# Optimization experiments

Measured on AMD Instinct MI355X. Metric: run time of the kernel, lower is better.

The kernel has to match this reference:

```python
import jax, jax.numpy as jnp
import numpy as np

N_RBF = 32
EPS_DIST = 0.01
R_RBF_MAX = 5.0
POWERS = (1.0, -1.0)


def _rbf_features(dist):
    # dist: [..., ] -> [..., N_RBF]; Gaussian-on-distance 'soft one-hot'
    q = jnp.linspace(0.0, 1.0, N_RBF).astype(dist.dtype)
    mu = q ** 2 * R_RBF_MAX
    sigma = (1.0 + R_RBF_MAX * q) / 7.0
    d = dist[..., None]
    return d ** 2 * jnp.exp(-d - ((d - mu) / sigma) ** 2)


def _pair_features(diff, dist):
    # RBF (32) + distance powers (2) + raw differences (3) = 37 features
    f_dist = jnp.stack(
        [dist ** n if n > 0 else 1.0 / (dist ** (-n) + EPS_DIST) for n in POWERS],
        axis=-1,
    )
    return jnp.concatenate([_rbf_features(dist), f_dist, diff], axis=-1)


def _mlp(x, Ws, bs):
    # MLP with linear_out=False: activation applied after every layer incl. last
    for W, b in zip(Ws, bs):
        x = jax.nn.silu(x @ W + b)
    return x


def setup_inputs() -> dict:
    key = jax.random.key(0)
    ks = jax.random.split(key, 6)
    B, N, M = 2048, 32, 8
    D_PAIR = N_RBF + 2 + 3  # 37
    H, F1, F_ION = 128, 128, 32
    r = jax.random.normal(ks[0], (B, N, 3), jnp.float32) * 2.0
    R = jax.random.normal(ks[1], (M, 3), jnp.float32) * 3.0
    Z = jnp.arange(1, M + 1, dtype=jnp.float32)
    init = lambda k, s: (jax.random.normal(k, s, jnp.float32) / np.sqrt(s[0])).astype(jnp.float32)
    return dict(
        r=r, R=R, Z=Z,
        W0=init(ks[2], (D_PAIR, H)), b0=jnp.zeros((H,), jnp.float32),
        W1=init(ks[3], (H, F1)), b1=jnp.zeros((F1,), jnp.float32),
        Wion=init(ks[4], (1, F_ION)), bion=jnp.zeros((F_ION,), jnp.float32),
    )


def reference(r, R, Z, W0, b0, W1, b1, Wion, bion):
    B, N = r.shape[0], r.shape[1]
    # --- pairwise diffs / distances ---
    diff_el_el = r[..., :, None, :] - r[..., None, :, :]          # [B,N,N,3]
    eye = jnp.eye(N, dtype=r.dtype)
    # safe sqrt on the diagonal (grad-safe), diagonal distance forced to 0
    dist_el_el = jnp.sqrt(jnp.sum(diff_el_el ** 2, axis=-1) + eye) * (1.0 - eye)  # [B,N,N]
    diff_el_ion = r[..., :, None, :] - R                           # [B,N,M,3]
    dist_el_ion = jnp.sqrt(jnp.sum(diff_el_ion ** 2, axis=-1))     # [B,N,M]

    # --- per-edge features ---
    features_el_el = _pair_features(diff_el_el, dist_el_el)        # [B,N,N,37]
    features_el_ion = _pair_features(diff_el_ion, dist_el_ion)     # [B,N,M,37]

    # --- edge MLP + sum aggregation over ions ---
    h = _mlp(features_el_ion, [W0, W1], [b0, b1])                  # [B,N,M,128]
    one_el = jnp.sum(h, axis=-2)                                   # [B,N,128]
    concat_ei = jnp.reshape(features_el_ion, features_el_ion.shape[:-2] + (-1,))  # [B,N,M*37]
    features_el = jnp.concatenate([one_el, concat_ei], axis=-1)    # [B,N,128+M*37]

    # --- ion features ---
    Zt = jnp.tile(Z, (B, 1))                                       # [B,M]
    features_ion = jax.nn.silu(Zt[..., None] @ Wion + bion)        # [B,M,32]
    return (features_el, features_ion)
```

## Files before the change

### kernel.cpp

```cpp
#include <hip/hip_runtime.h>


typedef __attribute__((ext_vector_type(8))) short short8;
typedef __attribute__((ext_vector_type(4))) float f32x4;

#define ITERS     8
#define UNITS_IT  16
#define ROWLEN    424
#define OUT_EL    27787264

__device__ __forceinline__ unsigned short f2bf(float f){
    unsigned int u = __builtin_bit_cast(unsigned int, f);
    u += 0x7fffu + ((u >> 16) & 1u);
    return (unsigned short)(u >> 16);
}
__device__ __forceinline__ unsigned int cvtpk_bf16(float lo, float hi){
    unsigned int r;
    asm("v_cvt_pk_bf16_f32 %0, %1, %2" : "=v"(r) : "v"(lo), "v"(hi));
    return r;
}
__device__ __forceinline__ unsigned short bf16s(float x){
    return (unsigned short)cvtpk_bf16(x, x);
}
__device__ __forceinline__ float fast_silu(float x){
    return x * __builtin_amdgcn_rcpf(1.0f + __expf(-x));
}

__global__ __launch_bounds__(512, 4)
void el_kernel(const float* __restrict__ r,
               const float* __restrict__ Rion,
               const float* __restrict__ W0,
               const float* __restrict__ b0,
               const float* __restrict__ W1,
               const float* __restrict__ b1,
               const float* __restrict__ Z,
               const float* __restrict__ Wion,
               const float* __restrict__ bion,
               float* __restrict__ out)
{
    __shared__ __align__(16) unsigned short W0L[8][2][64][8];
    __shared__ __align__(16) unsigned short W1L[8][4][64][8];
    __shared__ __align__(16) unsigned short UNI[8][2048];

    const int t    = threadIdx.x;
    const int lane = t & 63;
    const int w    = t >> 6;
    const int quad = lane >> 4;
    const int l16  = lane & 15;

    for (int i = t; i < 8*2*64*8; i += 512){
        int j = i & 7, ln = (i >> 3) & 63, ch = (i >> 9) & 1, tc = i >> 10;
        int q = ln >> 4, n = tc*16 + (ln & 15);
        float v = 0.f;
        if (ch == 0)            v = W0[(q*8 + j)*128 + n];
        else if (q == 0){
            if      (j < 5)     v = W0[(32 + j)*128 + n];
            else if (j == 5)    v = b0[n];
        }
        ((unsigned short*)W0L)[i] = f2bf(v);
    }
    for (int i = t; i < 8*4*64*8; i += 512){
        int j = i & 7, ln = (i >> 3) & 63, c = (i >> 9) & 3, tc = i >> 11;
        int k = c*32 + (ln >> 4)*8 + j, n = tc*16 + (ln & 15);
        ((unsigned short*)W1L)[i] = f2bf(W1[k*128 + n]);
    }
    if (t < 128){
        UNI[t >> 4][512 + (t & 15)*8 + 5] = 0x3F80;
        UNI[t >> 4][512 + (t & 15)*8 + 6] = 0;
        UNI[t >> 4][512 + (t & 15)*8 + 7] = 0;
    }

    {
        int e0 = (blockIdx.x*512 + t)*2;
        int j0 = e0 & 31, mm = (e0 >> 5) & 7;
        float z = Z[mm];
        float2 v;
        v.x = fast_silu(z * Wion[j0]     + bion[j0]);
        v.y = fast_silu(z * Wion[j0 + 1] + bion[j0 + 1]);
        *(float2*)&out[OUT_EL + e0] = v;
    }

    const int frow  = t >> 2;
    const int phase = t & 3;
    const int ul    = frow >> 3;
    const int m     = frow & 7;
    const int e16   = frow & 15;
    const float Rx = Rion[m*3+0];
    const float Ry = Rion[m*3+1];
    const float Rz = Rion[m*3+2];

    unsigned short* const uw = &UNI[w][0];
    const int h0row = l16 * 128;
    const int swz   = (l16 & 7) << 3;

    const f32x4 zeroc = {0.f,0.f,0.f,0.f};

    float bias1[8];
    #pragma unroll
    for (int tc = 0; tc < 8; ++tc) bias1[tc] = b1[tc*16 + l16];

    float muA[8], isA[8];
    #pragma unroll
    for (int k = 0; k < 8; ++k){
        float q = (float)(phase + 4*k) * (1.0f/31.0f);
        muA[k] = q*q*5.0f;
        isA[k] = 7.0f * __builtin_amdgcn_rcpf(1.0f + 5.0f*q);
    }

    const int ubase0 = blockIdx.x * (UNITS_IT * ITERS);

    float cx, cy, cz;
    {
        int gu = ubase0 + ul;
        cx = r[gu*3+0]; cy = r[gu*3+1]; cz = r[gu*3+2];
    }

    __syncthreads();

    for (int it = 0; it < ITERS; ++it){
        const int ubase = ubase0 + it * UNITS_IT;

        float nx = 0.f, ny = 0.f, nz = 0.f;
        if (it < ITERS-1){
            int gun = ubase + UNITS_IT + ul;
            nx = r[gun*3+0]; ny = r[gun*3+1]; nz = r[gun*3+2];
        }

        {
            int gu = ubase + ul;
            float dx = cx - Rx;
            float dy = cy - Ry;
            float dz = cz - Rz;
            float d2 = dx*dx + dy*dy + dz*dz;
            float d  = __builtin_amdgcn_sqrtf(d2);
            float* orow = &out[(size_t)gu*ROWLEN + 128 + m*37];
            #pragma unroll
            for (int k = 0; k < 8; ++k){
                float uu  = (d - muA[k]) * isA[k];
                float val = d2 * __expf(-d - uu*uu);
                orow[phase + 4*k] = val;
                uw[(k >> 1)*128 + e16*8 + phase + ((k & 1) << 2)] = bf16s(val);
            }
            if (phase == 0){
                orow[32] = d;  uw[512 + e16*8 + 0] = bf16s(d);
                orow[36] = dz; uw[512 + e16*8 + 4] = bf16s(dz);
            } else if (phase == 1){
                float v = __builtin_amdgcn_rcpf(d + 0.01f);
                orow[33] = v;  uw[512 + e16*8 + 1] = bf16s(v);
            } else if (phase == 2){
                orow[34] = dx; uw[512 + e16*8 + 2] = bf16s(dx);
            } else {
                orow[35] = dy; uw[512 + e16*8 + 3] = bf16s(dy);
                uw[512 + e16*8 + 5] = 0x3F80;
            }
        }

        short8 bf0 = *(const short8*)&uw[quad*128 + l16*8];
        short8 bf1 = *(const short8*)&uw[512 + l16*8];
        #pragma unroll
        for (int tc = 0; tc < 8; ++tc){
            short8 a0 = *(const short8*)&W0L[tc][0][lane][0];
            short8 a1 = *(const short8*)&W0L[tc][1][lane][0];
            f32x4 acc = __builtin_amdgcn_mfma_f32_16x16x32_bf16(a0, bf0, zeroc, 0, 0, 0);
            acc       = __builtin_amdgcn_mfma_f32_16x16x32_bf16(a1, bf1, acc,   0, 0, 0);
            unsigned int p01 = cvtpk_bf16(fast_silu(acc[0]), fast_silu(acc[1]));
            unsigned int p23 = cvtpk_bf16(fast_silu(acc[2]), fast_silu(acc[3]));
            unsigned long long pk = (unsigned long long)p01 |
                                    ((unsigned long long)p23 << 32);
            *(unsigned long long*)&uw[h0row + ((tc*16 + quad*4) ^ swz)] = pk;
        }

        short8 afk[4];
        #pragma unroll
        for (int c = 0; c < 4; ++c)
            afk[c] = *(const short8*)&uw[h0row + ((c*32 + quad*8) ^ swz)];

        f32x4 acc1[8];
        #pragma unroll
        for (int i = 0; i < 8; ++i) acc1[i] = zeroc;
        __builtin_amdgcn_s_setprio(1);
        #pragma unroll
        for (int c = 0; c < 4; ++c){
            #pragma unroll
            for (int tc = 0; tc < 8; ++tc){
                short8 bw = *(const short8*)&W1L[tc][c][lane][0];
                acc1[tc] = __builtin_amdgcn_mfma_f32_16x16x32_bf16(afk[c], bw, acc1[tc], 0, 0, 0);
            }
        }
        __builtin_amdgcn_s_setprio(0);
        #pragma unroll
        for (int tc = 0; tc < 8; ++tc){
            float v = 0.f;
            #pragma unroll
            for (int rr = 0; rr < 4; ++rr) v += fast_silu(acc1[tc][rr] + bias1[tc]);
            v += __shfl_xor(v, 16, 64);
            if ((quad & 1) == 0){
                size_t gu = (size_t)(ubase + 2*w + (quad >> 1));
                out[gu*ROWLEN + tc*16 + l16] = v;
            }
        }

        cx = nx; cy = ny; cz = nz;
    }
}

extern "C" void kernel_launch(void* const* d_in, const int* in_sizes, int n_in,
                              void* d_out, int out_size, void* d_ws, size_t ws_size,
                              hipStream_t stream)
{
    const float* r    = (const float*)d_in[0];
    const float* Rion = (const float*)d_in[1];
    const float* Z    = (const float*)d_in[2];
    const float* W0   = (const float*)d_in[3];
    const float* b0   = (const float*)d_in[4];
    const float* W1   = (const float*)d_in[5];
    const float* b1   = (const float*)d_in[6];
    const float* Wion = (const float*)d_in[7];
    const float* bion = (const float*)d_in[8];
    float* out = (float*)d_out;

    el_kernel<<<dim3(512), dim3(512), 0, stream>>>(r, Rion, W0, b0, W1, b1,
                                                   Z, Wion, bion, out);
}
```

Baseline: 181.6 us.

## Double block size and stream hidden layer in chunks to shrink LDS

Blocks grow to 1024 threads (16 waves), with 32 units per iteration over 4 iterations. The two MLP layers are interleaved per 32-column chunk, so each chunk of the first-layer output goes through a small per-wave LDS scratch and straight into the second-layer MFMAs. This cuts the per-wave LDS buffer from 2048 to 640 shorts. The RBF constants are recomputed inline instead of being kept in registers, and the ion-feature tail now writes one element per thread. The aim is higher occupancy and less LDS and register use, at the cost of a tighter register budget from the new launch bounds (possible spills) and a scratch area that overlaps the feature staging region.

```diff
diff --git a/kernel.cpp b/kernel.cpp
--- a/kernel.cpp
+++ b/kernel.cpp
@@ -4,8 +4,8 @@
 typedef __attribute__((ext_vector_type(8))) short short8;
 typedef __attribute__((ext_vector_type(4))) float f32x4;
 
-#define ITERS     8
-#define UNITS_IT  16
+#define ITERS     4
+#define UNITS_IT  32
 #define ROWLEN    424
 #define OUT_EL    27787264
 
@@ -26,7 +26,7 @@
     return x * __builtin_amdgcn_rcpf(1.0f + __expf(-x));
 }
 
-__global__ __launch_bounds__(512, 4)
+__global__ __launch_bounds__(1024, 8)
 void el_kernel(const float* __restrict__ r,
                const float* __restrict__ Rion,
                const float* __restrict__ W0,
@@ -40,7 +40,7 @@
 {
     __shared__ __align__(16) unsigned short W0L[8][2][64][8];
     __shared__ __align__(16) unsigned short W1L[8][4][64][8];
-    __shared__ __align__(16) unsigned short UNI[8][2048];
+    __shared__ __align__(16) unsigned short UNI[16][640];
 
     const int t    = threadIdx.x;
     const int lane = t & 63;
@@ -48,7 +48,7 @@
     const int quad = lane >> 4;
     const int l16  = lane & 15;
 
-    for (int i = t; i < 8*2*64*8; i += 512){
+    for (int i = t; i < 8*2*64*8; i += 1024){
         int j = i & 7, ln = (i >> 3) & 63, ch = (i >> 9) & 1, tc = i >> 10;
         int q = ln >> 4, n = tc*16 + (ln & 15);
         float v = 0.f;
@@ -59,25 +59,21 @@
         }
         ((unsigned short*)W0L)[i] = f2bf(v);
     }
-    for (int i = t; i < 8*4*64*8; i += 512){
+    for (int i = t; i < 8*4*64*8; i += 1024){
         int j = i & 7, ln = (i >> 3) & 63, c = (i >> 9) & 3, tc = i >> 11;
         int k = c*32 + (ln >> 4)*8 + j, n = tc*16 + (ln & 15);
         ((unsigned short*)W1L)[i] = f2bf(W1[k*128 + n]);
     }
-    if (t < 128){
+    if (t < 256){
         UNI[t >> 4][512 + (t & 15)*8 + 5] = 0x3F80;
         UNI[t >> 4][512 + (t & 15)*8 + 6] = 0;
         UNI[t >> 4][512 + (t & 15)*8 + 7] = 0;
     }
 
     {
-        int e0 = (blockIdx.x*512 + t)*2;
-        int j0 = e0 & 31, mm = (e0 >> 5) & 7;
-        float z = Z[mm];
-        float2 v;
-        v.x = fast_silu(z * Wion[j0]     + bion[j0]);
-        v.y = fast_silu(z * Wion[j0 + 1] + bion[j0 + 1]);
-        *(float2*)&out[OUT_EL + e0] = v;
+        int e = blockIdx.x*1024 + t;
+        int j = e & 31, mm = (e >> 5) & 7;
+        out[OUT_EL + e] = fast_silu(Z[mm] * Wion[j] + bion[j]);
     }
 
     const int frow  = t >> 2;
@@ -90,22 +86,12 @@
     const float Rz = Rion[m*3+2];
 
     unsigned short* const uw = &UNI[w][0];
-    const int h0row = l16 * 128;
-    const int swz   = (l16 & 7) << 3;
 
     const f32x4 zeroc = {0.f,0.f,0.f,0.f};
 
     float bias1[8];
     #pragma unroll
     for (int tc = 0; tc < 8; ++tc) bias1[tc] = b1[tc*16 + l16];
-
-    float muA[8], isA[8];
-    #pragma unroll
-    for (int k = 0; k < 8; ++k){
-        float q = (float)(phase + 4*k) * (1.0f/31.0f);
-        muA[k] = q*q*5.0f;
-        isA[k] = 7.0f * __builtin_amdgcn_rcpf(1.0f + 5.0f*q);
-    }
 
     const int ubase0 = blockIdx.x * (UNITS_IT * ITERS);
 
@@ -136,7 +122,10 @@
             float* orow = &out[(size_t)gu*ROWLEN + 128 + m*37];
             #pragma unroll
             for (int k = 0; k < 8; ++k){
-                float uu  = (d - muA[k]) * isA[k];
+                float q   = (float)(phase + 4*k) * (1.0f/31.0f);
+                float mu  = q*q*5.0f;
+                float is  = 7.0f * __builtin_amdgcn_rcpf(1.0f + 5.0f*q);
+                float uu  = (d - mu) * is;
                 float val = d2 * __expf(-d - uu*uu);
                 orow[phase + 4*k] = val;
                 uw[(k >> 1)*128 + e16*8 + phase + ((k & 1) << 2)] = bf16s(val);
@@ -157,37 +146,35 @@
 
         short8 bf0 = *(const short8*)&uw[quad*128 + l16*8];
         short8 bf1 = *(const short8*)&uw[512 + l16*8];
-        #pragma unroll
-        for (int tc = 0; tc < 8; ++tc){
-            short8 a0 = *(const short8*)&W0L[tc][0][lane][0];
-            short8 a1 = *(const short8*)&W0L[tc][1][lane][0];
-            f32x4 acc = __builtin_amdgcn_mfma_f32_16x16x32_bf16(a0, bf0, zeroc, 0, 0, 0);
-            acc       = __builtin_amdgcn_mfma_f32_16x16x32_bf16(a1, bf1, acc,   0, 0, 0);
-            unsigned int p01 = cvtpk_bf16(fast_silu(acc[0]), fast_silu(acc[1]));
-            unsigned int p23 = cvtpk_bf16(fast_silu(acc[2]), fast_silu(acc[3]));
-            unsigned long long pk = (unsigned long long)p01 |
-                                    ((unsigned long long)p23 << 32);
-            *(unsigned long long*)&uw[h0row + ((tc*16 + quad*4) ^ swz)] = pk;
-        }
-
-        short8 afk[4];
-        #pragma unroll
-        for (int c = 0; c < 4; ++c)
-            afk[c] = *(const short8*)&uw[h0row + ((c*32 + quad*8) ^ swz)];
-
         f32x4 acc1[8];
         #pragma unroll
         for (int i = 0; i < 8; ++i) acc1[i] = zeroc;
-        __builtin_amdgcn_s_setprio(1);
+
         #pragma unroll
         for (int c = 0; c < 4; ++c){
             #pragma unroll
-            for (int tc = 0; tc < 8; ++tc){
-                short8 bw = *(const short8*)&W1L[tc][c][lane][0];
-                acc1[tc] = __builtin_amdgcn_mfma_f32_16x16x32_bf16(afk[c], bw, acc1[tc], 0, 0, 0);
-            }
-        }
-        __builtin_amdgcn_s_setprio(0);
+            for (int h = 0; h < 2; ++h){
+                const int tc = 2*c + h;
+                short8 a0 = *(const short8*)&W0L[tc][0][lane][0];
+                short8 a1 = *(const short8*)&W0L[tc][1][lane][0];
+                f32x4 acc = __builtin_amdgcn_mfma_f32_16x16x32_bf16(a0, bf0, zeroc, 0, 0, 0);
+                acc       = __builtin_amdgcn_mfma_f32_16x16x32_bf16(a1, bf1, acc,   0, 0, 0);
+                unsigned int p01 = cvtpk_bf16(fast_silu(acc[0]), fast_silu(acc[1]));
+                unsigned int p23 = cvtpk_bf16(fast_silu(acc[2]), fast_silu(acc[3]));
+                unsigned long long pk = (unsigned long long)p01 |
+                                        ((unsigned long long)p23 << 32);
+                *(unsigned long long*)&uw[l16*40 + h*16 + quad*4] = pk;
+            }
+            short8 afk = *(const short8*)&uw[l16*40 + quad*8];
+            __builtin_amdgcn_s_setprio(1);
+            #pragma unroll
+            for (int tc2 = 0; tc2 < 8; ++tc2){
+                short8 bw = *(const short8*)&W1L[tc2][c][lane][0];
+                acc1[tc2] = __builtin_amdgcn_mfma_f32_16x16x32_bf16(afk, bw, acc1[tc2], 0, 0, 0);
+            }
+            __builtin_amdgcn_s_setprio(0);
+        }
+
         #pragma unroll
         for (int tc = 0; tc < 8; ++tc){
             float v = 0.f;
@@ -219,6 +206,6 @@
     const float* bion = (const float*)d_in[8];
     float* out = (float*)d_out;
 
-    el_kernel<<<dim3(512), dim3(512), 0, stream>>>(r, Rion, W0, b0, W1, b1,
-                                                   Z, Wion, bion, out);
-}
+    el_kernel<<<dim3(512), dim3(1024), 0, stream>>>(r, Rion, W0, b0, W1, b1,
+                                                    Z, Wion, bion, out);
+}
```

Result: slower. 252.8 us (+39.2%).

## Double-buffer edge features and interleave layer-0 chunks with layer-1 MFMAs

Applied to the files above, without the earlier changes.

Edge features for the next iteration's units are now computed into a second per-wave LDS buffer while the current iteration's MLP runs, forming a one-stage software pipeline. The first layer's hidden activations are no longer all materialized before layer 1. Instead, each 32-wide k-chunk is produced and immediately consumed by the layer-1 MFMAs, which shrinks the LDS scratch per wave. The aim is to overlap the exp-heavy feature math and its global stores with MFMA work, at the cost of one redundant feature pass per block on the wrapped final iteration and a different register and LDS schedule.

```diff
diff --git a/kernel.cpp b/kernel.cpp
--- a/kernel.cpp
+++ b/kernel.cpp
@@ -40,7 +40,7 @@
 {
     __shared__ __align__(16) unsigned short W0L[8][2][64][8];
     __shared__ __align__(16) unsigned short W1L[8][4][64][8];
-    __shared__ __align__(16) unsigned short UNI[8][2048];
+    __shared__ __align__(16) unsigned short UNI[8][1920];
 
     const int t    = threadIdx.x;
     const int lane = t & 63;
@@ -65,9 +65,13 @@
         ((unsigned short*)W1L)[i] = f2bf(W1[k*128 + n]);
     }
     if (t < 128){
-        UNI[t >> 4][512 + (t & 15)*8 + 5] = 0x3F80;
-        UNI[t >> 4][512 + (t & 15)*8 + 6] = 0;
-        UNI[t >> 4][512 + (t & 15)*8 + 7] = 0;
+        int ww = t >> 4, e = t & 15;
+        #pragma unroll
+        for (int b = 0; b < 2; ++b){
+            UNI[ww][b*640 + 512 + e*8 + 5] = 0x3F80;
+            UNI[ww][b*640 + 512 + e*8 + 6] = 0;
+            UNI[ww][b*640 + 512 + e*8 + 7] = 0;
+        }
     }
 
     {
@@ -90,8 +94,6 @@
     const float Rz = Rion[m*3+2];
 
     unsigned short* const uw = &UNI[w][0];
-    const int h0row = l16 * 128;
-    const int swz   = (l16 & 7) << 3;
 
     const f32x4 zeroc = {0.f,0.f,0.f,0.f};
 
@@ -101,93 +103,91 @@
 
     float muA[8], isA[8];
     #pragma unroll
-    for (int k = 0; k < 8; ++k){
-        float q = (float)(phase + 4*k) * (1.0f/31.0f);
-        muA[k] = q*q*5.0f;
-        isA[k] = 7.0f * __builtin_amdgcn_rcpf(1.0f + 5.0f*q);
+    for (int kk = 0; kk < 8; ++kk){
+        float q = (float)(phase + 4*kk) * (1.0f/31.0f);
+        muA[kk] = q*q*5.0f;
+        isA[kk] = 7.0f * __builtin_amdgcn_rcpf(1.0f + 5.0f*q);
     }
 
     const int ubase0 = blockIdx.x * (UNITS_IT * ITERS);
 
+    auto feat_pass = [&](int gu, int fb, float px, float py, float pz){
+        float dx = px - Rx, dy = py - Ry, dz = pz - Rz;
+        float d2 = dx*dx + dy*dy + dz*dz;
+        float d  = __builtin_amdgcn_sqrtf(d2);
+        float* orow = &out[(size_t)gu*ROWLEN + 128 + m*37];
+        #pragma unroll
+        for (int kk = 0; kk < 8; ++kk){
+            float uu  = (d - muA[kk]) * isA[kk];
+            float val = d2 * __expf(-d - uu*uu);
+            orow[phase + 4*kk] = val;
+            uw[fb + (kk >> 1)*128 + e16*8 + phase + ((kk & 1) << 2)] = bf16s(val);
+        }
+        float tv = (phase == 0) ? d :
+                   (phase == 1) ? __builtin_amdgcn_rcpf(d + 0.01f) :
+                   (phase == 2) ? dx : dy;
+        orow[32 + phase] = tv;
+        orow[36]         = dz;
+        uw[fb + 512 + e16*8 + phase] = bf16s(tv);
+        uw[fb + 512 + e16*8 + 4]     = bf16s(dz);
+    };
+
+    {
+        int gu = ubase0 + ul;
+        feat_pass(gu, 0, r[gu*3+0], r[gu*3+1], r[gu*3+2]);
+    }
     float cx, cy, cz;
     {
-        int gu = ubase0 + ul;
+        int gu = ubase0 + UNITS_IT + ul;
         cx = r[gu*3+0]; cy = r[gu*3+1]; cz = r[gu*3+2];
     }
 
     __syncthreads();
 
+    int cur = 0;
     for (int it = 0; it < ITERS; ++it){
         const int ubase = ubase0 + it * UNITS_IT;
 
-        float nx = 0.f, ny = 0.f, nz = 0.f;
-        if (it < ITERS-1){
-            int gun = ubase + UNITS_IT + ul;
-            nx = r[gun*3+0]; ny = r[gun*3+1]; nz = r[gun*3+2];
-        }
+        int gun = ubase0 + (((it + 2) & (ITERS-1)) * UNITS_IT) + ul;
+        float nx = r[gun*3+0], ny = r[gun*3+1], nz = r[gun*3+2];
+
+        short8 bf0 = *(const short8*)&uw[cur + quad*128 + l16*8];
+        short8 bf1 = *(const short8*)&uw[cur + 512 + l16*8];
 
         {
-            int gu = ubase + ul;
-            float dx = cx - Rx;
-            float dy = cy - Ry;
-            float dz = cz - Rz;
-            float d2 = dx*dx + dy*dy + dz*dz;
-            float d  = __builtin_amdgcn_sqrtf(d2);
-            float* orow = &out[(size_t)gu*ROWLEN + 128 + m*37];
-            #pragma unroll
-            for (int k = 0; k < 8; ++k){
-                float uu  = (d - muA[k]) * isA[k];
-                float val = d2 * __expf(-d - uu*uu);
-                orow[phase + 4*k] = val;
-                uw[(k >> 1)*128 + e16*8 + phase + ((k & 1) << 2)] = bf16s(val);
-            }
-            if (phase == 0){
-                orow[32] = d;  uw[512 + e16*8 + 0] = bf16s(d);
-                orow[36] = dz; uw[512 + e16*8 + 4] = bf16s(dz);
-            } else if (phase == 1){
-                float v = __builtin_amdgcn_rcpf(d + 0.01f);
-                orow[33] = v;  uw[512 + e16*8 + 1] = bf16s(v);
-            } else if (phase == 2){
-                orow[34] = dx; uw[512 + e16*8 + 2] = bf16s(dx);
-            } else {
-                orow[35] = dy; uw[512 + e16*8 + 3] = bf16s(dy);
-                uw[512 + e16*8 + 5] = 0x3F80;
-            }
-        }
-
-        short8 bf0 = *(const short8*)&uw[quad*128 + l16*8];
-        short8 bf1 = *(const short8*)&uw[512 + l16*8];
-        #pragma unroll
-        for (int tc = 0; tc < 8; ++tc){
-            short8 a0 = *(const short8*)&W0L[tc][0][lane][0];
-            short8 a1 = *(const short8*)&W0L[tc][1][lane][0];
-            f32x4 acc = __builtin_amdgcn_mfma_f32_16x16x32_bf16(a0, bf0, zeroc, 0, 0, 0);
-            acc       = __builtin_amdgcn_mfma_f32_16x16x32_bf16(a1, bf1, acc,   0, 0, 0);
-            unsigned int p01 = cvtpk_bf16(fast_silu(acc[0]), fast_silu(acc[1]));
-            unsigned int p23 = cvtpk_bf16(fast_silu(acc[2]), fast_silu(acc[3]));
-            unsigned long long pk = (unsigned long long)p01 |
-                                    ((unsigned long long)p23 << 32);
-            *(unsigned long long*)&uw[h0row + ((tc*16 + quad*4) ^ swz)] = pk;
-        }
-
-        short8 afk[4];
-        #pragma unroll
-        for (int c = 0; c < 4; ++c)
-            afk[c] = *(const short8*)&uw[h0row + ((c*32 + quad*8) ^ swz)];
+            int gu = ubase0 + (((it + 1) & (ITERS-1)) * UNITS_IT) + ul;
+            feat_pass(gu, cur ^ 640, cx, cy, cz);
+        }
 
         f32x4 acc1[8];
         #pragma unroll
         for (int i = 0; i < 8; ++i) acc1[i] = zeroc;
-        __builtin_amdgcn_s_setprio(1);
+
         #pragma unroll
         for (int c = 0; c < 4; ++c){
             #pragma unroll
-            for (int tc = 0; tc < 8; ++tc){
-                short8 bw = *(const short8*)&W1L[tc][c][lane][0];
-                acc1[tc] = __builtin_amdgcn_mfma_f32_16x16x32_bf16(afk[c], bw, acc1[tc], 0, 0, 0);
+            for (int h = 0; h < 2; ++h){
+                const int tc = 2*c + h;
+                short8 a0 = *(const short8*)&W0L[tc][0][lane][0];
+                short8 a1 = *(const short8*)&W0L[tc][1][lane][0];
+                f32x4 acc = __builtin_amdgcn_mfma_f32_16x16x32_bf16(a0, bf0, zeroc, 0, 0, 0);
+                acc       = __builtin_amdgcn_mfma_f32_16x16x32_bf16(a1, bf1, acc,   0, 0, 0);
+                unsigned int p01 = cvtpk_bf16(fast_silu(acc[0]), fast_silu(acc[1]));
+                unsigned int p23 = cvtpk_bf16(fast_silu(acc[2]), fast_silu(acc[3]));
+                unsigned long long pk = (unsigned long long)p01 |
+                                        ((unsigned long long)p23 << 32);
+                *(unsigned long long*)&uw[1280 + l16*40 + h*16 + quad*4] = pk;
             }
-        }
-        __builtin_amdgcn_s_setprio(0);
+            short8 afk = *(const short8*)&uw[1280 + l16*40 + quad*8];
+            __builtin_amdgcn_s_setprio(1);
+            #pragma unroll
+            for (int tc2 = 0; tc2 < 8; ++tc2){
+                short8 bw = *(const short8*)&W1L[tc2][c][lane][0];
+                acc1[tc2] = __builtin_amdgcn_mfma_f32_16x16x32_bf16(afk, bw, acc1[tc2], 0, 0, 0);
+            }
+            __builtin_amdgcn_s_setprio(0);
+        }
+
         #pragma unroll
         for (int tc = 0; tc < 8; ++tc){
             float v = 0.f;
@@ -200,6 +200,7 @@
             }
         }
 
+        cur ^= 640;
         cx = nx; cy = ny; cz = nz;
     }
 }
```

Result: no change. 181.8 us (+0.1%).
